# Performance work log

Measured on AMD Instinct MI355X. Metric: run time of the kernel, lower is better.

The kernel has to match this reference:

```python
import jax, jax.numpy as jnp
import numpy as np

N_HEADS = 4
IN_FEATURES = 1024


def setup_inputs() -> dict:
    key = jax.random.key(0)
    ks = jax.random.split(key, 20)
    B, HW, C = 2, 16384, 1024
    inp = {
        "q": jax.random.normal(ks[0], (B, HW, C), dtype=jnp.float32),
        "k": jax.random.normal(ks[1], (B, HW, C), dtype=jnp.float32),
        "v": jax.random.normal(ks[2], (B, HW, C), dtype=jnp.float32),
    }
    names = ["wqg", "bqg", "wkg", "bkg", "wvg", "bvg",
             "wql", "bql", "wkl", "bkl", "wvl", "bvl", "wp", "bp"]
    for i, n in enumerate(names):
        inp[n] = jax.random.normal(ks[3 + i], (C,), dtype=jnp.float32)
    return inp


def _channel_attention(qm, km, vm, scale):
    # qm/km/vm: (b, hw, c). Attention over the CHANNEL dim per head.
    b, n, c = qm.shape
    d = c // N_HEADS
    qh = qm.reshape(b, n, N_HEADS, d).transpose(0, 2, 3, 1)  # (b, H, d, hw)
    kh = km.reshape(b, n, N_HEADS, d).transpose(0, 2, 3, 1)
    vh = vm.reshape(b, n, N_HEADS, d).transpose(0, 2, 3, 1)
    scores = jnp.einsum("bhdn,bhen->bhde", qh, kh) * scale  # (b, H, d, d)
    attn = jax.nn.softmax(scores, axis=-1)
    out = jnp.einsum("bhde,bhen->bhdn", attn, vh)            # (b, H, d, hw)
    return out.transpose(0, 3, 1, 2).reshape(b, n, c)        # (b, hw, c)


def reference(q, k, v, wqg, bqg, wkg, bkg, wvg, bvg,
              wql, bql, wkl, bkl, wvl, bvl, wp, bp):
    scale = IN_FEATURES ** (-0.5)
    # Depthwise (groups==channels, kernel=1) projections: per-channel affine.
    att_global = _channel_attention(q * wqg + bqg, k * wkg + bkg, v * wvg + bvg, scale)
    # window_size=1 -> local patch extraction is identity; local branch uses its own maps.
    att_local = _channel_attention(q * wql + bql, k * wkl + bkl, v * wvl + bvl, scale)
    att = att_global + att_local
    # Both accumulators hold the same att, so projection input is 2*att.
    return (2.0 * att) * wp + bp
```

## Files before the change

kernel.cpp:

```cpp
#include <hip/hip_runtime.h>
#include <stdint.h>

#define NTOK 16384
#define CDIM 1024
#define DHEAD 256

typedef short s16x8 __attribute__((ext_vector_type(8)));
typedef unsigned short u16x8 __attribute__((ext_vector_type(8)));
typedef _Float16 h16x8 __attribute__((ext_vector_type(8)));
typedef float f32x4 __attribute__((ext_vector_type(4)));
typedef float f32x16 __attribute__((ext_vector_type(16)));

static __device__ __forceinline__ unsigned short f2bf(float f) {
    union { float f; unsigned u; } x; x.f = f;
    unsigned r = (x.u + 0x7fffu + ((x.u >> 16) & 1u)) >> 16;
    return (unsigned short)r;
}
static __device__ __forceinline__ unsigned short f2h(float f) {
    _Float16 h = (_Float16)f;
    return __builtin_bit_cast(unsigned short, h);
}
static __device__ __forceinline__ unsigned cvtpk(float lo, float hi) {
    unsigned r;
    asm("v_cvt_pk_bf16_f32 %0, %1, %2" : "=v"(r) : "v"(lo), "v"(hi));
    return r;
}
static __device__ __forceinline__ void lgkm_barrier() {
    asm volatile("s_waitcnt lgkmcnt(0)" ::: "memory");
    __builtin_amdgcn_s_barrier();
}

__global__ __launch_bounds__(512, 2)
void k_gram(const float* __restrict__ q, const float* __restrict__ k,
            unsigned short* __restrict__ Gpart, float* __restrict__ Spart, int nchunk)
{
    __shared__ __align__(16) unsigned short ls[2 * DHEAD * 32];
    unsigned short* lq = ls;
    unsigned short* lk = ls + DHEAD * 32;

    const int t     = threadIdx.x;
    const int bh    = blockIdx.x & 7;
    const int chunk = blockIdx.x >> 3;
    const int b     = bh >> 2, h = bh & 3;
    const int rows  = NTOK / nchunk;
    const int S     = rows >> 5;
    const int n0c   = chunk * rows;

    const int lane = t & 63, w = t >> 6;
    const int isK  = t >> 8;
    const int tl   = t & 255;
    const int ng   = tl & 3;
    const int ch0  = (tl >> 2) * 4;
    const int de0  = (w >> 1) * 64;
    const int e0   = (w & 1) * 128;

    const float* src    = isK ? k : q;
    unsigned short* dst = isK ? lk : lq;
    const float* row0 = src + ((size_t)b * NTOK + n0c + ng * 8) * CDIM + (size_t)h * DHEAD + ch0;

    f32x4 vA[4], vB[4];
#define GL_A(sidx) do { const size_t o_ = (size_t)(sidx) * 32 * CDIM;                \
        _Pragma("unroll") for (int j_ = 0; j_ < 4; ++j_)                              \
            vA[j_] = *reinterpret_cast<const f32x4*>(row0 + o_ + (size_t)j_ * CDIM);   \
        asm volatile("" ::: "memory"); } while (0)
#define GL_B(sidx) do { const size_t o_ = (size_t)(sidx) * 32 * CDIM + 4 * CDIM;     \
        _Pragma("unroll") for (int j_ = 0; j_ < 4; ++j_)                              \
            vB[j_] = *reinterpret_cast<const f32x4*>(row0 + o_ + (size_t)j_ * CDIM);   \
        asm volatile("" ::: "memory"); } while (0)

    GL_A(0);
    GL_B(0);

    float ssum[4] = {0.f, 0.f, 0.f, 0.f};
    f32x4 acc[4][8];
#pragma unroll
    for (int r = 0; r < 4; ++r)
#pragma unroll
        for (int c = 0; c < 8; ++c) acc[r][c] = (f32x4){0.f, 0.f, 0.f, 0.f};

    for (int s = 0; s < S; ++s) {
#pragma unroll
        for (int c = 0; c < 4; ++c) {
            const int ch = ch0 + c;
            ushort4 p;
            p.x = f2bf(vA[0][c]); p.y = f2bf(vA[1][c]);
            p.z = f2bf(vA[2][c]); p.w = f2bf(vA[3][c]);
            ssum[c] += (vA[0][c] + vA[1][c]) + (vA[2][c] + vA[3][c]);
            *reinterpret_cast<ushort4*>(&dst[ch * 32 + ((ng ^ ((ch >> 1) & 3)) * 8)]) = p;
        }
        if (s + 1 < S) GL_A(s + 1);

#pragma unroll
        for (int c = 0; c < 4; ++c) {
            const int ch = ch0 + c;
            ushort4 p;
            p.x = f2bf(vB[0][c]); p.y = f2bf(vB[1][c]);
            p.z = f2bf(vB[2][c]); p.w = f2bf(vB[3][c]);
            ssum[c] += (vB[0][c] + vB[1][c]) + (vB[2][c] + vB[3][c]);
            *reinterpret_cast<ushort4*>(&dst[ch * 32 + ((ng ^ ((ch >> 1) & 3)) * 8) + 4]) = p;
        }
        if (s + 1 < S) GL_B(s + 1);

        lgkm_barrier();

        {
            s16x8 af[4], bfr[8];
            const int slot = lane >> 4;
#pragma unroll
            for (int r = 0; r < 4; ++r) {
                const int row = de0 + r * 16 + (lane & 15);
                af[r] = *reinterpret_cast<const s16x8*>(&lq[row * 32 + ((slot ^ ((row >> 1) & 3)) * 8)]);
            }
#pragma unroll
            for (int c = 0; c < 8; ++c) {
                const int row = e0 + c * 16 + (lane & 15);
                bfr[c] = *reinterpret_cast<const s16x8*>(&lk[row * 32 + ((slot ^ ((row >> 1) & 3)) * 8)]);
            }
#pragma unroll
            for (int r = 0; r < 4; ++r)
#pragma unroll
                for (int c = 0; c < 8; ++c)
                    acc[r][c] = __builtin_amdgcn_mfma_f32_16x16x32_bf16(af[r], bfr[c], acc[r][c], 0, 0, 0);
        }
        lgkm_barrier();
    }
#undef GL_A
#undef GL_B

#pragma unroll
    for (int off = 1; off < 4; off <<= 1)
#pragma unroll
        for (int c = 0; c < 4; ++c) ssum[c] += __shfl_xor(ssum[c], off);
    if ((lane & 3) == 0) {
        float* sp = Spart + (size_t)(bh * nchunk + chunk) * 512 + isK * 256;
        *reinterpret_cast<float4*>(&sp[ch0]) = make_float4(ssum[0], ssum[1], ssum[2], ssum[3]);
    }

    unsigned short* gp = Gpart + (size_t)(bh * nchunk + chunk) * 65536;
#pragma unroll
    for (int qtr = 0; qtr < 4; ++qtr) {
        if ((w >> 1) == qtr) {
#pragma unroll
            for (int r = 0; r < 4; ++r) {
                const int de_l = r * 16 + (lane >> 4) * 4;
#pragma unroll
                for (int c = 0; c < 8; ++c) {
                    const int e = e0 + c * 16 + (lane & 15);
#pragma unroll
                    for (int reg = 0; reg < 4; ++reg)
                        ls[(de_l + reg) * 256 + e] = f2h(acc[r][c][reg]);
                }
            }
        }
        lgkm_barrier();
#pragma unroll
        for (int i = 0; i < 4; ++i) {
            const int idx = i * 512 + t;
            *reinterpret_cast<u16x8*>(gp + qtr * 16384 + idx * 8) =
                *reinterpret_cast<const u16x8*>(&ls[idx * 8]);
        }
        lgkm_barrier();
    }
}

__global__ __launch_bounds__(256)
void k_scores(const unsigned short* __restrict__ Gpart, const float* __restrict__ Spart,
              const float* __restrict__ wqg, const float* __restrict__ bqg,
              const float* __restrict__ wkg, const float* __restrict__ bkg,
              const float* __restrict__ wvg, const float* __restrict__ bvg,
              const float* __restrict__ wql, const float* __restrict__ bql,
              const float* __restrict__ wkl, const float* __restrict__ bkl,
              const float* __restrict__ wvl, const float* __restrict__ bvl,
              const float* __restrict__ wp,  const float* __restrict__ bp,
              unsigned short* __restrict__ Wf, float* __restrict__ beta, int nchunk)
{
    __shared__ float sSq[256], sSk[256];
    const int t  = threadIdx.x;
    const int bh = blockIdx.x >> 5;
    const int rg = blockIdx.x & 31;
    const int h  = bh & 3;

    float aq = 0.f, ak = 0.f;
    for (int c = 0; c < nchunk; ++c) {
        const float* sp = Spart + (size_t)(bh * nchunk + c) * 512;
        aq += sp[t]; ak += sp[256 + t];
    }
    sSq[t] = aq; sSk[t] = ak;
    __syncthreads();

    const int dl  = t >> 5;
    const int de  = rg * 8 + dl;
    const int e8  = (t & 31) * 8;
    const int cd  = h * DHEAD + de;
    const int ce0 = h * DHEAD + e8;

    float g[8] = {0.f, 0.f, 0.f, 0.f, 0.f, 0.f, 0.f, 0.f};
    const unsigned short* gpb = Gpart + (size_t)bh * nchunk * 65536 + (size_t)de * 256 + e8;
    for (int c = 0; c < nchunk; ++c) {
        h16x8 v = *reinterpret_cast<const h16x8*>(gpb + (size_t)c * 65536);
#pragma unroll
        for (int j = 0; j < 8; ++j) g[j] += (float)v[j];
    }

    const float sqv = sSq[de];
    float skv[8];
#pragma unroll
    for (int j = 0; j < 8; ++j) skv[j] = sSk[e8 + j];

    float wrow[8] = {0.f, 0.f, 0.f, 0.f, 0.f, 0.f, 0.f, 0.f};
    float bacc = 0.f;
    const float scale = 0.03125f;
#pragma unroll
    for (int br = 0; br < 2; ++br) {
        const float* wq = br ? wql : wqg;  const float* bq = br ? bql : bqg;
        const float* wk = br ? wkl : wkg;  const float* bk = br ? bkl : bkg;
        const float* wv = br ? wvl : wvg;  const float* bv = br ? bvl : bvg;
        const float wqv = wq[cd], bqv = bq[cd];

        float s[8], mm = -1e30f;
#pragma unroll
        for (int j = 0; j < 8; ++j) {
            const float wkv = wk[ce0 + j], bkv = bk[ce0 + j];
            s[j] = scale * (wqv * wkv * g[j] + wqv * bkv * sqv
                            + bqv * wkv * skv[j] + bqv * bkv * 16384.0f);
            mm = fmaxf(mm, s[j]);
        }
#pragma unroll
        for (int off = 16; off; off >>= 1) mm = fmaxf(mm, __shfl_xor(mm, off));
        float p[8], sum = 0.f;
#pragma unroll
        for (int j = 0; j < 8; ++j) { p[j] = __expf(s[j] - mm); sum += p[j]; }
#pragma unroll
        for (int off = 16; off; off >>= 1) sum += __shfl_xor(sum, off);
        const float inv = 1.f / sum;
#pragma unroll
        for (int j = 0; j < 8; ++j) {
            const float a = p[j] * inv;
            wrow[j] += a * wv[ce0 + j];
            bacc    += a * bv[ce0 + j];
        }
    }
    const float wp2 = 2.f * wp[cd];
    u16x8 pw;
#pragma unroll
    for (int j = 0; j < 8; ++j) pw[j] = f2bf(wp2 * wrow[j]);
    *reinterpret_cast<u16x8*>(Wf + (size_t)bh * 65536 + (size_t)de * 256 + e8) = pw;
#pragma unroll
    for (int off = 16; off; off >>= 1) bacc += __shfl_xor(bacc, off);
    if ((t & 31) == 0) beta[bh * 256 + de] = wp2 * bacc + bp[cd];
}

__global__ __launch_bounds__(256, 2)
void k_out(const float* __restrict__ v, const unsigned short* __restrict__ Wf,
           const float* __restrict__ beta, float* __restrict__ out)
{
    const int P    = blockIdx.x;
    const int bh   = P & 7;
    const int tile = P >> 3;
    const int b    = bh >> 2, h = bh & 3;

    const int t = threadIdx.x;
    const int w = t >> 6, lane = t & 63;
    const int l31 = lane & 31, g2 = lane >> 5;
    const int n0 = tile * 128 + w * 32;

    const float* pv = v + (size_t)(b * NTOK + n0 + l31) * CDIM + h * DHEAD + g2 * 8;
    const unsigned short* pw = Wf + (size_t)bh * 65536 + (size_t)l31 * 256 + g2 * 8;

    f32x4 Aa[2], Ab[2];
    u16x8 Ba[8], Bb[8];

#define LDSTEP(av, bv2, ks) do {                                              \
        av[0] = *reinterpret_cast<const f32x4*>(pv + (ks) * 16);               \
        av[1] = *reinterpret_cast<const f32x4*>(pv + (ks) * 16 + 4);           \
        _Pragma("unroll") for (int dg = 0; dg < 8; ++dg)                       \
            bv2[dg] = *reinterpret_cast<const u16x8*>(pw + (size_t)dg * 8192 + (ks) * 16); \
    } while (0)

    f32x16 acc[8];
#pragma unroll
    for (int dg = 0; dg < 8; ++dg)
#pragma unroll
        for (int j = 0; j < 16; ++j) acc[dg][j] = 0.f;

#define CPSTEP(av, bv2) do {                                                  \
        int4 A;                                                               \
        A.x = cvtpk(av[0][0], av[0][1]); A.y = cvtpk(av[0][2], av[0][3]);     \
        A.z = cvtpk(av[1][0], av[1][1]); A.w = cvtpk(av[1][2], av[1][3]);     \
        const s16x8 fA = __builtin_bit_cast(s16x8, A);                        \
        _Pragma("unroll") for (int dg = 0; dg < 8; ++dg)                      \
            acc[dg] = __builtin_amdgcn_mfma_f32_32x32x16_bf16(                \
                fA, __builtin_bit_cast(s16x8, bv2[dg]), acc[dg], 0, 0, 0);    \
    } while (0)

    LDSTEP(Aa, Ba, 0);
#pragma unroll
    for (int ks = 0; ks < 16; ks += 2) {
        if (ks + 1 < 16) LDSTEP(Ab, Bb, ks + 1);
        CPSTEP(Aa, Ba);
        if (ks + 2 < 16) LDSTEP(Aa, Ba, ks + 2);
        if (ks + 1 < 16) CPSTEP(Ab, Bb);
    }
#undef LDSTEP
#undef CPSTEP

#pragma unroll
    for (int dg = 0; dg < 8; ++dg) {
        const float bb = beta[bh * 256 + dg * 32 + l31];
#pragma unroll
        for (int reg = 0; reg < 16; ++reg) {
            const int row = (reg & 3) + 8 * (reg >> 2) + 4 * g2;
            out[(size_t)(b * NTOK + n0 + row) * CDIM + h * DHEAD + dg * 32 + l31] =
                acc[dg][reg] + bb;
        }
    }
}

extern "C" void kernel_launch(void* const* d_in, const int* in_sizes, int n_in,
                              void* d_out, int out_size, void* d_ws, size_t ws_size,
                              hipStream_t stream)
{
    const float* q = (const float*)d_in[0];
    const float* k = (const float*)d_in[1];
    const float* v = (const float*)d_in[2];
    const float* wgt[14];
    for (int i = 0; i < 14; ++i) wgt[i] = (const float*)d_in[3 + i];
    float* out = (float*)d_out;

    int nchunk = 32;
    while (nchunk > 1) {
        size_t need = (size_t)8 * nchunk * 65536 * 2
                    + (size_t)8 * nchunk * 512 * 4
                    + (size_t)8 * 65536 * 2
                    + (size_t)8 * 256 * 4 + 1024;
        if (need <= ws_size) break;
        nchunk >>= 1;
    }

    char* p = (char*)d_ws;
    unsigned short* Gpart = (unsigned short*)p; p += (size_t)8 * nchunk * 65536 * 2;
    float* Spart = (float*)p;                   p += (size_t)8 * nchunk * 512 * 4;
    unsigned short* Wf = (unsigned short*)p;    p += (size_t)8 * 65536 * 2;
    float* beta  = (float*)p;

    k_gram<<<dim3(8 * nchunk), dim3(512), 0, stream>>>(q, k, Gpart, Spart, nchunk);
    k_scores<<<dim3(8 * 32), dim3(256), 0, stream>>>(
        Gpart, Spart,
        wgt[0], wgt[1], wgt[2], wgt[3], wgt[4], wgt[5],
        wgt[6], wgt[7], wgt[8], wgt[9], wgt[10], wgt[11],
        wgt[12], wgt[13], Wf, beta, nchunk);
    k_out<<<dim3(8 * 128), dim3(256), 0, stream>>>(v, Wf, beta, out);
}
```

Baseline: 193.9 us.

## Stage projection weights in swizzled LDS and split output columns across blocks

```diff
diff --git a/kernel.cpp b/kernel.cpp
--- a/kernel.cpp
+++ b/kernel.cpp
@@ -254,64 +254,79 @@
 void k_out(const float* __restrict__ v, const unsigned short* __restrict__ Wf,
            const float* __restrict__ beta, float* __restrict__ out)
 {
+    __shared__ __align__(16) unsigned short lw[128 * 256];
     const int P    = blockIdx.x;
     const int bh   = P & 7;
-    const int tile = P >> 3;
+    const int rest = P >> 3;
+    const int tile = rest >> 1;
+    const int ddh  = rest & 1;
     const int b    = bh >> 2, h = bh & 3;
+    const int n0   = tile * 128;
 
     const int t = threadIdx.x;
     const int w = t >> 6, lane = t & 63;
     const int l31 = lane & 31, g2 = lane >> 5;
-    const int n0 = tile * 128 + w * 32;
-
-    const float* pv = v + (size_t)(b * NTOK + n0 + l31) * CDIM + h * DHEAD + g2 * 8;
-    const unsigned short* pw = Wf + (size_t)bh * 65536 + (size_t)l31 * 256 + g2 * 8;
+
+    {
+        const unsigned short* ws = Wf + (size_t)bh * 65536 + (size_t)(ddh * 128) * 256;
+#pragma unroll
+        for (int p = 0; p < 16; ++p) {
+            const int row = p * 8 + (t >> 5);
+            const int c8  = t & 31;
+            const u16x8 val = *reinterpret_cast<const u16x8*>(ws + (size_t)row * 256 + c8 * 8);
+            *reinterpret_cast<u16x8*>(&lw[row * 256 + ((c8 ^ (row & 31)) * 8)]) = val;
+        }
+    }
+    __syncthreads();
+
+    const float* pv = v + (size_t)(b * NTOK + n0 + w * 32 + l31) * CDIM + h * DHEAD + g2 * 8;
 
     f32x4 Aa[2], Ab[2];
-    u16x8 Ba[8], Bb[8];
-
-#define LDSTEP(av, bv2, ks) do {                                              \
+#define LDSTEP(av, ks) do {                                                   \
         av[0] = *reinterpret_cast<const f32x4*>(pv + (ks) * 16);               \
         av[1] = *reinterpret_cast<const f32x4*>(pv + (ks) * 16 + 4);           \
-        _Pragma("unroll") for (int dg = 0; dg < 8; ++dg)                       \
-            bv2[dg] = *reinterpret_cast<const u16x8*>(pw + (size_t)dg * 8192 + (ks) * 16); \
     } while (0)
 
-    f32x16 acc[8];
-#pragma unroll
-    for (int dg = 0; dg < 8; ++dg)
-#pragma unroll
-        for (int j = 0; j < 16; ++j) acc[dg][j] = 0.f;
-
-#define CPSTEP(av, bv2) do {                                                  \
+    f32x16 acc[4];
+#pragma unroll
+    for (int dgl = 0; dgl < 4; ++dgl)
+#pragma unroll
+        for (int j = 0; j < 16; ++j) acc[dgl][j] = 0.f;
+
+#define CPSTEP(av, ks) do {                                                   \
         int4 A;                                                               \
         A.x = cvtpk(av[0][0], av[0][1]); A.y = cvtpk(av[0][2], av[0][3]);     \
         A.z = cvtpk(av[1][0], av[1][1]); A.w = cvtpk(av[1][2], av[1][3]);     \
         const s16x8 fA = __builtin_bit_cast(s16x8, A);                        \
-        _Pragma("unroll") for (int dg = 0; dg < 8; ++dg)                      \
-            acc[dg] = __builtin_amdgcn_mfma_f32_32x32x16_bf16(                \
-                fA, __builtin_bit_cast(s16x8, bv2[dg]), acc[dg], 0, 0, 0);    \
-    } while (0)
-
-    LDSTEP(Aa, Ba, 0);
+        const int sg = (ks) * 2 + g2;                                         \
+        _Pragma("unroll") for (int dgl = 0; dgl < 4; ++dgl) {                 \
+            const int row = dgl * 32 + l31;                                   \
+            const s16x8 fB = *reinterpret_cast<const s16x8*>(                 \
+                &lw[row * 256 + ((sg ^ (row & 31)) * 8)]);                    \
+            acc[dgl] = __builtin_amdgcn_mfma_f32_32x32x16_bf16(               \
+                fA, fB, acc[dgl], 0, 0, 0);                                   \
+        } } while (0)
+
+    LDSTEP(Aa, 0);
 #pragma unroll
     for (int ks = 0; ks < 16; ks += 2) {
-        if (ks + 1 < 16) LDSTEP(Ab, Bb, ks + 1);
-        CPSTEP(Aa, Ba);
-        if (ks + 2 < 16) LDSTEP(Aa, Ba, ks + 2);
-        if (ks + 1 < 16) CPSTEP(Ab, Bb);
+        if (ks + 1 < 16) LDSTEP(Ab, ks + 1);
+        CPSTEP(Aa, ks);
+        if (ks + 2 < 16) LDSTEP(Aa, ks + 2);
+        if (ks + 1 < 16) CPSTEP(Ab, ks + 1);
     }
 #undef LDSTEP
 #undef CPSTEP
 
 #pragma unroll
-    for (int dg = 0; dg < 8; ++dg) {
-        const float bb = beta[bh * 256 + dg * 32 + l31];
+    for (int dgl = 0; dgl < 4; ++dgl) {
+        const int dd = ddh * 128 + dgl * 32 + l31;
+        const float bb = beta[bh * 256 + dd];
 #pragma unroll
         for (int reg = 0; reg < 16; ++reg) {
             const int row = (reg & 3) + 8 * (reg >> 2) + 4 * g2;
-            out[(size_t)(b * NTOK + n0 + row) * CDIM + h * DHEAD + dg * 32 + l31] =
-                acc[dg][reg] + bb;
+            out[(size_t)(b * NTOK + n0 + w * 32 + row) * CDIM + h * DHEAD + dd] =
+                acc[dgl][reg] + bb;
         }
     }
 }
@@ -349,5 +364,5 @@
         wgt[0], wgt[1], wgt[2], wgt[3], wgt[4], wgt[5],
         wgt[6], wgt[7], wgt[8], wgt[9], wgt[10], wgt[11],
         wgt[12], wgt[13], Wf, beta, nchunk);
-    k_out<<<dim3(8 * 128), dim3(256), 0, stream>>>(v, Wf, beta, out);
-}
+    k_out<<<dim3(8 * 256), dim3(256), 0, stream>>>(v, Wf, beta, out);
+}
```

Result: faster. 158.8 us (-18.1%).
